# Kernel tuning notes

Measured on AMD Instinct MI355X. Metric: run time of the kernel, lower is better.

## Reference

```python
import jax, jax.numpy as jnp
import numpy as np

B, S, D, A = 8, 4096, 128, 128


def _pos_encoding(seq_len, dim):
    # sin/cos positional encoding, same construction as the torch buffer
    pos = np.arange(seq_len, dtype=np.float32)[:, None]
    div = np.exp(np.arange(0, dim, 2, dtype=np.float32) * (-np.log(10000.0) / dim))
    pe = np.zeros((seq_len, dim), dtype=np.float32)
    pe[:, 0::2] = np.sin(pos * div)
    pe[:, 1::2] = np.cos(pos * div)
    return jnp.asarray(pe)


def setup_inputs() -> dict:
    key = jax.random.key(0)
    ks = jax.random.split(key, 7)
    sc = 1.0 / np.sqrt(D)
    return {
        "x": jax.random.normal(ks[0], (B, S, D), dtype=jnp.float32),
        "Wq": jax.random.normal(ks[1], (D, A), dtype=jnp.float32) * sc,
        "bq": jnp.zeros((A,), dtype=jnp.float32),
        "Wk": jax.random.normal(ks[2], (D, A), dtype=jnp.float32) * sc,
        "bk": jnp.zeros((A,), dtype=jnp.float32),
        "Wv": jax.random.normal(ks[3], (D, A), dtype=jnp.float32) * sc,
        "bv": jnp.zeros((A,), dtype=jnp.float32),
    }


def reference(x, Wq, bq, Wk, bk, Wv, bv):
    b, s, d = x.shape
    pe = _pos_encoding(s, d)  # [S, D]
    xp = x + pe[None]  # broadcast add of positional encoding
    q = xp @ Wq + bq  # [B, S, A]
    k = xp @ Wk + bk
    v = xp @ Wv + bv
    scale = 1.0 / jnp.sqrt(jnp.asarray(Wq.shape[1], dtype=jnp.float32))
    scores = jnp.einsum("bsa,bta->bst", q, k) * scale  # [B, S, S]
    weights = jax.nn.softmax(scores, axis=-1)
    out = jnp.einsum("bst,bta->bsa", weights, v)  # [B, S, A]
    return out
```

## Files before the change

kernel.cpp:

```cpp
#include <hip/hip_runtime.h>

#define BB 8
#define SS 4096
#define DD 128

typedef __attribute__((ext_vector_type(8))) short v8s;
typedef __attribute__((ext_vector_type(4))) short v4s;
typedef __attribute__((ext_vector_type(4))) float v4f;

__device__ __forceinline__ unsigned short f2bf(float f) {
    unsigned int u = __float_as_uint(f);
    u += 0x7fffu + ((u >> 16) & 1u);
    return (unsigned short)(u >> 16);
}
__device__ __forceinline__ float bf2f(unsigned short s) {
    return __uint_as_float(((unsigned int)s) << 16);
}
__device__ __forceinline__ unsigned int pk_bf16(float a, float b) {
    unsigned int ua = __float_as_uint(a) + 0x8000u;
    unsigned int ub = __float_as_uint(b) + 0x8000u;
    return __builtin_amdgcn_perm(ub, ua, 0x07060302u);
}

#if !defined(__HIP_DEVICE_COMPILE__)
#define MFMA_BF16_32(a, b, c) (c)
#else
#define MFMA_BF16_32(a, b, c) __builtin_amdgcn_mfma_f32_16x16x32_bf16((a), (b), (c), 0, 0, 0)
#endif

#if !defined(__HIP_DEVICE_COMPILE__)
#define EXP2F(x) exp2f(x)
#elif __has_builtin(__builtin_amdgcn_exp2f)
#define EXP2F(x) __builtin_amdgcn_exp2f(x)
#else
#define EXP2F(x) exp2f(x)
#endif

#define QSCALE 0.12751743f
#define FIXM 24.0f

__global__ __launch_bounds__(256) void prep_w_kernel(
    const float* __restrict__ Wq, const float* __restrict__ Wk,
    const float* __restrict__ Wv, unsigned short* __restrict__ Wt)
{
    int id = blockIdx.x * 256 + threadIdx.x;
    int w = id >> 14;
    int n = (id >> 7) & 127;
    int k = id & 127;
    const float* W = (w == 0) ? Wq : (w == 1) ? Wk : Wv;
    Wt[id] = f2bf(W[k * 128 + n]);
}

__global__ __launch_bounds__(256) void proj_kernel(
    const float* __restrict__ x, const unsigned short* __restrict__ Wt,
    const float* __restrict__ bq, const float* __restrict__ bk,
    const float* __restrict__ bv,
    unsigned short* __restrict__ qo, unsigned short* __restrict__ ko,
    unsigned short* __restrict__ vo)
{
    __shared__ __attribute__((aligned(16))) unsigned short o_lds[9216];

    const int tid = threadIdx.x;
    const int wave = tid >> 6;
    const int lane = tid & 63;
    const int quad = lane >> 4;
    const int l15 = lane & 15;
    const int bid = blockIdx.x;
    const int mat = bid % 3;
    const int rbase = (bid / 3) * 64;

    const int flatrow = rbase + wave * 16 + l15;
    const int srow = flatrow & 4095;
    v8s af[4];
#pragma unroll
    for (int kc = 0; kc < 4; ++kc) {
        const int kbase = kc * 32 + quad * 8;
        const v4f* xp = (const v4f*)(x + (size_t)flatrow * DD + kbase);
        v4f x0 = xp[0], x1 = xp[1];
        float xv[8] = {x0[0], x0[1], x0[2], x0[3], x1[0], x1[1], x1[2], x1[3]};
        v8s a;
#pragma unroll
        for (int j = 0; j < 8; ++j) {
            int d = kbase + j;
            float freq = __expf((float)(d & ~1) * -0.07195578415606394f);
            float arg = (float)srow * freq;
            float pe = (d & 1) ? __cosf(arg) : __sinf(arg);
            a[j] = (short)f2bf(xv[j] + pe);
        }
        af[kc] = a;
    }

    const unsigned short* Wp = Wt + (mat << 14);
    const float* bias = (mat == 0) ? bq : (mat == 1) ? bk : bv;

#pragma unroll
    for (int nb = 0; nb < 8; ++nb) {
        const int col = nb * 16 + l15;
        v4f acc = {0.f, 0.f, 0.f, 0.f};
#pragma unroll
        for (int kc = 0; kc < 4; ++kc) {
            v8s bf = *(const v8s*)(Wp + col * 128 + kc * 32 + quad * 8);
            acc = MFMA_BF16_32(af[kc], bf, acc);
        }
        float bval = bias[col];
#pragma unroll
        for (int reg = 0; reg < 4; ++reg) {
            int lr = wave * 16 + quad * 4 + reg;
            float val = acc[reg] + bval;
            if (mat == 0) {
                o_lds[lr * 136 + col] = f2bf(val * QSCALE);
            } else if (mat == 1) {
                o_lds[lr * 136 + col] = f2bf(val);
            } else {
                o_lds[col * 72 + lr] = f2bf(val);
            }
        }
    }
    __syncthreads();

    if (mat <= 1) {
        unsigned short* outp = (mat == 0) ? qo : ko;
#pragma unroll
        for (int it = 0; it < 4; ++it) {
            int id = it * 256 + tid;
            int r = id >> 4, c8 = id & 15;
            *(v8s*)(outp + (size_t)(rbase + r) * DD + c8 * 8) =
                *(const v8s*)(o_lds + r * 136 + c8 * 8);
        }
    } else {
        const int b0 = rbase >> 12, s0 = rbase & 4095;
#pragma unroll
        for (int it = 0; it < 4; ++it) {
            int id = it * 256 + tid;
            int a = id >> 3, c = id & 7;
            *(v8s*)(vo + ((size_t)(b0 * 128 + a)) * SS + s0 + c * 8) =
                *(const v8s*)(o_lds + a * 72 + c * 8);
        }
    }
}

#define HKEYS 2048
#define NT (HKEYS / 64)
__global__ __launch_bounds__(256, 2) void flash_kernel(
    const unsigned short* __restrict__ qg,
    const unsigned short* __restrict__ kg,
    const unsigned short* __restrict__ vg,
    float* __restrict__ out,
    unsigned short* __restrict__ o2,
    float* __restrict__ statl)
{
    __shared__ __attribute__((aligned(16))) unsigned short k_lds[2][8192];
    __shared__ __attribute__((aligned(16))) unsigned short v_lds[2][8192];

    const int tid = threadIdx.x;
    const int wave = tid >> 6;
    const int lane = tid & 63;
    const int quad = lane >> 4;
    const int l15 = lane & 15;
    const int bid = blockIdx.x;
    const int b = bid & 7;
    const int half = (bid >> 3) & 1;
    const int qt = bid >> 4;
    const int qbase = qt * 128 + wave * 32;

    v8s qfA[4], qfB[4];
    {
        const size_t rA = (size_t)(b * SS + qbase + l15) * DD;
        const size_t rB = (size_t)(b * SS + qbase + 16 + l15) * DD;
#pragma unroll
        for (int kc = 0; kc < 4; ++kc) {
            qfA[kc] = *(const v8s*)(qg + rA + kc * 32 + quad * 8);
            qfB[kc] = *(const v8s*)(qg + rB + kc * 32 + quad * 8);
        }
    }

    v4f oA[8], oB[8];
#pragma unroll
    for (int i = 0; i < 8; ++i) {
        oA[i] = (v4f){0.f, 0.f, 0.f, 0.f};
        oB[i] = (v4f){0.f, 0.f, 0.f, 0.f};
    }
    v4f laccA = {0.f, 0.f, 0.f, 0.f}, laccB = {0.f, 0.f, 0.f, 0.f};

    v8s ones;
#pragma unroll
    for (int j = 0; j < 8; ++j) ones[j] = (short)0x3F80;

    const unsigned short* kb = kg + (size_t)b * SS * DD + (size_t)half * HKEYS * DD;
    const unsigned short* vb = vg + (size_t)b * DD * SS + half * HKEYS;

    int kbo[4], vbo[2][2];
#pragma unroll
    for (int kc = 0; kc < 4; ++kc)
        kbo[kc] = l15 * 128 + (((kc * 4 + quad) ^ (l15 & 7)) << 3);
#pragma unroll
    for (int kc2 = 0; kc2 < 2; ++kc2) {
        vbo[kc2][0] = l15 * 64 + (((kc2 * 8 + quad) ^ l15) << 2);
        vbo[kc2][1] = l15 * 64 + (((kc2 * 8 + 4 + quad) ^ l15) << 2);
    }
    const int kr_r = tid >> 4, kr_c = tid & 15;
    const int va0 = tid >> 3, vc4 = (tid & 7) * 2;
    const int kwb = kr_r * 128 + ((kr_c ^ (kr_r & 7)) << 3);
    const int vwb0 = va0 * 64 + ((vc4 ^ (va0 & 15)) << 2);
    const int vwb1 = va0 * 64 + (((vc4 + 1) ^ (va0 & 15)) << 2);

    v8s kr[4], vr[4];
    auto load_tile = [&](int t) {
        const unsigned short* kp = kb + (size_t)t * 64 * DD;
        const unsigned short* vp = vb + t * 64;
#pragma unroll
        for (int it = 0; it < 4; ++it) {
            kr[it] = *(const v8s*)(kp + (size_t)(kr_r + it * 16) * DD + kr_c * 8);
            vr[it] = *(const v8s*)(vp + (size_t)(va0 + it * 32) * SS + (tid & 7) * 8);
        }
    };
    auto store_tile = [&](int p) {
#pragma unroll
        for (int it = 0; it < 4; ++it) {
            *(v8s*)(&k_lds[p][kwb + it * 2048]) = kr[it];
            v4s lo = {vr[it][0], vr[it][1], vr[it][2], vr[it][3]};
            v4s hi = {vr[it][4], vr[it][5], vr[it][6], vr[it][7]};
            *(v4s*)(&v_lds[p][vwb0 + it * 2048]) = lo;
            *(v4s*)(&v_lds[p][vwb1 + it * 2048]) = hi;
        }
    };
    auto compute = [&](int p) {
        v4f sA[4], sB[4];
#pragma unroll
        for (int c = 0; c < 4; ++c) {
            v4f aA = {0.f, 0.f, 0.f, 0.f};
            v4f aB = {0.f, 0.f, 0.f, 0.f};
#pragma unroll
            for (int kc = 0; kc < 4; ++kc) {
                v8s af = *(const v8s*)(&k_lds[p][c * 2048 + kbo[kc]]);
                aA = MFMA_BF16_32(af, qfA[kc], aA);
                aB = MFMA_BF16_32(af, qfB[kc], aB);
            }
            sA[c] = aA;
            sB[c] = aB;
        }
        union { v8s v[2]; unsigned int u[8]; } PA, PB;
#pragma unroll
        for (int c = 0; c < 4; ++c) {
            float a0 = EXP2F(sA[c][0] - FIXM), a1 = EXP2F(sA[c][1] - FIXM);
            float a2 = EXP2F(sA[c][2] - FIXM), a3 = EXP2F(sA[c][3] - FIXM);
            PA.u[c * 2]     = pk_bf16(a0, a1);
            PA.u[c * 2 + 1] = pk_bf16(a2, a3);
            float b0 = EXP2F(sB[c][0] - FIXM), b1 = EXP2F(sB[c][1] - FIXM);
            float b2 = EXP2F(sB[c][2] - FIXM), b3 = EXP2F(sB[c][3] - FIXM);
            PB.u[c * 2]     = pk_bf16(b0, b1);
            PB.u[c * 2 + 1] = pk_bf16(b2, b3);
        }
#pragma unroll
        for (int kc2 = 0; kc2 < 2; ++kc2) {
            laccA = MFMA_BF16_32(PA.v[kc2], ones, laccA);
            laccB = MFMA_BF16_32(PB.v[kc2], ones, laccB);
#pragma unroll
            for (int ab = 0; ab < 8; ++ab) {
                union { v8s v; v4s h[2]; } bf;
                bf.h[0] = *(const v4s*)(&v_lds[p][ab * 1024 + vbo[kc2][0]]);
                bf.h[1] = *(const v4s*)(&v_lds[p][ab * 1024 + vbo[kc2][1]]);
                oA[ab] = MFMA_BF16_32(PA.v[kc2], bf.v, oA[ab]);
                oB[ab] = MFMA_BF16_32(PB.v[kc2], bf.v, oB[ab]);
            }
        }
    };

    load_tile(0);
    store_tile(0);
    load_tile(1);
    __syncthreads();
#pragma unroll 1
    for (int kt = 0; kt < NT; kt += 2) {
        store_tile(1);
        if (kt + 2 < NT) load_tile(kt + 2);
        compute(0);
        __syncthreads();
        if (kt + 2 < NT) {
            store_tile(0);
            if (kt + 3 < NT) load_tile(kt + 3);
        }
        compute(1);
        __syncthreads();
    }

    if (l15 == 0) {
        int qi = half * (BB * SS) + b * SS + qbase;
#pragma unroll
        for (int reg = 0; reg < 4; ++reg) {
            statl[qi + quad * 4 + reg] = laccA[reg];
            statl[qi + 16 + quad * 4 + reg] = laccB[reg];
        }
    }
#pragma unroll
    for (int ab = 0; ab < 8; ++ab)
#pragma unroll
        for (int reg = 0; reg < 4; ++reg) {
            int srA = qbase + quad * 4 + reg;
            size_t iA = (size_t)(b * SS + srA) * DD + ab * 16 + l15;
            size_t iB = (size_t)(b * SS + srA + 16) * DD + ab * 16 + l15;
            if (half == 0) {
                out[iA] = oA[ab][reg];
                out[iB] = oB[ab][reg];
            } else {
                o2[iA] = f2bf(oA[ab][reg]);
                o2[iB] = f2bf(oB[ab][reg]);
            }
        }
}

__global__ __launch_bounds__(256) void combine_kernel(
    float* __restrict__ out, const unsigned short* __restrict__ o2,
    const float* __restrict__ statl)
{
    int id = blockIdx.x * 256 + threadIdx.x;
    int row = id >> 5;
    int c = (id & 31) * 4;
    float l1 = statl[row], l2 = statl[BB * SS + row];
    float inv = 1.0f / (l1 + l2);
    size_t base = (size_t)row * DD + c;
    v4f o1 = *(v4f*)(out + base);
    v4s p2 = *(const v4s*)(o2 + base);
    v4f r;
#pragma unroll
    for (int j = 0; j < 4; ++j)
        r[j] = (o1[j] + bf2f((unsigned short)p2[j])) * inv;
    *(v4f*)(out + base) = r;
}

extern "C" void kernel_launch(void* const* d_in, const int* in_sizes, int n_in,
                              void* d_out, int out_size, void* d_ws, size_t ws_size,
                              hipStream_t stream)
{
    const float* x  = (const float*)d_in[0];
    const float* Wq = (const float*)d_in[1];
    const float* bq = (const float*)d_in[2];
    const float* Wk = (const float*)d_in[3];
    const float* bk = (const float*)d_in[4];
    const float* Wv = (const float*)d_in[5];
    const float* bv = (const float*)d_in[6];
    float* out = (float*)d_out;

    unsigned short* Wt = (unsigned short*)d_ws;
    unsigned short* q  = Wt + 49152;
    unsigned short* k  = q + (size_t)BB * SS * DD;
    unsigned short* vT = k + (size_t)BB * SS * DD;
    unsigned short* O2 = vT + (size_t)BB * SS * DD;
    float* statl = (float*)(O2 + (size_t)BB * SS * DD);

    hipLaunchKernelGGL(prep_w_kernel, dim3(192), dim3(256), 0, stream, Wq, Wk, Wv, Wt);
    hipLaunchKernelGGL(proj_kernel, dim3(BB * SS / 64 * 3), dim3(256), 0, stream,
                       x, Wt, bq, bk, bv, q, k, vT);
    hipLaunchKernelGGL(flash_kernel, dim3(SS / 128 * 2 * BB), dim3(256), 0, stream,
                       q, k, vT, out, O2, statl);
    hipLaunchKernelGGL(combine_kernel, dim3(BB * SS * DD / 4 / 256), dim3(256), 0, stream,
                       out, O2, statl);
}
```

Before: 187.1 us.

## Use 32x32x16 MFMA in flash attention and fuse QKV projection per block

The flash kernel moves from 16x16x32 MFMAs over 64-key tiles to 32x32x16 MFMAs over 32-key tiles. Each wave now holds one 32-row query fragment and sums row exponentials in registers with a shuffle, replacing the ones-vector MFMA used for the denominator. The projection kernel computes Q, K and V in one block, so the positional-encoded x fragment is built once instead of three times. The cost is a larger LDS footprint in the projection kernel and shorter key tiles, which means more barriers per key in the flash loop.

```diff
diff --git a/kernel.cpp b/kernel.cpp
--- a/kernel.cpp
+++ b/kernel.cpp
@@ -7,6 +7,7 @@
 typedef __attribute__((ext_vector_type(8))) short v8s;
 typedef __attribute__((ext_vector_type(4))) short v4s;
 typedef __attribute__((ext_vector_type(4))) float v4f;
+typedef __attribute__((ext_vector_type(16))) float v16f;
 
 __device__ __forceinline__ unsigned short f2bf(float f) {
     unsigned int u = __float_as_uint(f);
@@ -23,9 +24,11 @@
 }
 
 #if !defined(__HIP_DEVICE_COMPILE__)
-#define MFMA_BF16_32(a, b, c) (c)
+#define MFMA16(a, b, c) (c)
+#define MFMA32(a, b, c) (c)
 #else
-#define MFMA_BF16_32(a, b, c) __builtin_amdgcn_mfma_f32_16x16x32_bf16((a), (b), (c), 0, 0, 0)
+#define MFMA16(a, b, c) __builtin_amdgcn_mfma_f32_16x16x32_bf16((a), (b), (c), 0, 0, 0)
+#define MFMA32(a, b, c) __builtin_amdgcn_mfma_f32_32x32x16_bf16((a), (b), (c), 0, 0, 0)
 #endif
 
 #if !defined(__HIP_DEVICE_COMPILE__)
@@ -51,23 +54,23 @@
     Wt[id] = f2bf(W[k * 128 + n]);
 }
 
-__global__ __launch_bounds__(256) void proj_kernel(
+__global__ __launch_bounds__(256, 3) void proj_kernel(
     const float* __restrict__ x, const unsigned short* __restrict__ Wt,
     const float* __restrict__ bq, const float* __restrict__ bk,
     const float* __restrict__ bv,
     unsigned short* __restrict__ qo, unsigned short* __restrict__ ko,
     unsigned short* __restrict__ vo)
 {
-    __shared__ __attribute__((aligned(16))) unsigned short o_lds[9216];
+    __shared__ __attribute__((aligned(16))) unsigned short o_q[64 * 136];
+    __shared__ __attribute__((aligned(16))) unsigned short o_k[64 * 136];
+    __shared__ __attribute__((aligned(16))) unsigned short o_v[128 * 72];
 
     const int tid = threadIdx.x;
     const int wave = tid >> 6;
     const int lane = tid & 63;
     const int quad = lane >> 4;
     const int l15 = lane & 15;
-    const int bid = blockIdx.x;
-    const int mat = bid % 3;
-    const int rbase = (bid / 3) * 64;
+    const int rbase = blockIdx.x * 64;
 
     const int flatrow = rbase + wave * 16 + l15;
     const int srow = flatrow & 4095;
@@ -90,57 +93,58 @@
         af[kc] = a;
     }
 
-    const unsigned short* Wp = Wt + (mat << 14);
-    const float* bias = (mat == 0) ? bq : (mat == 1) ? bk : bv;
-
-#pragma unroll
-    for (int nb = 0; nb < 8; ++nb) {
-        const int col = nb * 16 + l15;
-        v4f acc = {0.f, 0.f, 0.f, 0.f};
-#pragma unroll
-        for (int kc = 0; kc < 4; ++kc) {
-            v8s bf = *(const v8s*)(Wp + col * 128 + kc * 32 + quad * 8);
-            acc = MFMA_BF16_32(af[kc], bf, acc);
-        }
-        float bval = bias[col];
-#pragma unroll
-        for (int reg = 0; reg < 4; ++reg) {
-            int lr = wave * 16 + quad * 4 + reg;
-            float val = acc[reg] + bval;
-            if (mat == 0) {
-                o_lds[lr * 136 + col] = f2bf(val * QSCALE);
-            } else if (mat == 1) {
-                o_lds[lr * 136 + col] = f2bf(val);
-            } else {
-                o_lds[col * 72 + lr] = f2bf(val);
+#pragma unroll
+    for (int mat = 0; mat < 3; ++mat) {
+        const unsigned short* Wp = Wt + (mat << 14);
+        const float* bias = (mat == 0) ? bq : (mat == 1) ? bk : bv;
+#pragma unroll
+        for (int nb = 0; nb < 8; ++nb) {
+            const int col = nb * 16 + l15;
+            v4f acc = {0.f, 0.f, 0.f, 0.f};
+#pragma unroll
+            for (int kc = 0; kc < 4; ++kc) {
+                v8s bf = *(const v8s*)(Wp + col * 128 + kc * 32 + quad * 8);
+                acc = MFMA16(af[kc], bf, acc);
             }
+            float bval = bias[col];
+#pragma unroll
+            for (int reg = 0; reg < 4; ++reg) {
+                int lr = wave * 16 + quad * 4 + reg;
+                float val = acc[reg] + bval;
+                if (mat == 0) {
+                    o_q[lr * 136 + col] = f2bf(val * QSCALE);
+                } else if (mat == 1) {
+                    o_k[lr * 136 + col] = f2bf(val);
+                } else {
+                    o_v[col * 72 + lr] = f2bf(val);
+                }
+            }
         }
     }
     __syncthreads();
 
-    if (mat <= 1) {
-        unsigned short* outp = (mat == 0) ? qo : ko;
-#pragma unroll
-        for (int it = 0; it < 4; ++it) {
-            int id = it * 256 + tid;
-            int r = id >> 4, c8 = id & 15;
-            *(v8s*)(outp + (size_t)(rbase + r) * DD + c8 * 8) =
-                *(const v8s*)(o_lds + r * 136 + c8 * 8);
-        }
-    } else {
-        const int b0 = rbase >> 12, s0 = rbase & 4095;
-#pragma unroll
-        for (int it = 0; it < 4; ++it) {
-            int id = it * 256 + tid;
-            int a = id >> 3, c = id & 7;
-            *(v8s*)(vo + ((size_t)(b0 * 128 + a)) * SS + s0 + c * 8) =
-                *(const v8s*)(o_lds + a * 72 + c * 8);
-        }
-    }
-}
-
+#pragma unroll
+    for (int it = 0; it < 4; ++it) {
+        int id = it * 256 + tid;
+        int r = id >> 4, c8 = id & 15;
+        *(v8s*)(qo + (size_t)(rbase + r) * DD + c8 * 8) =
+            *(const v8s*)(o_q + r * 136 + c8 * 8);
+        *(v8s*)(ko + (size_t)(rbase + r) * DD + c8 * 8) =
+            *(const v8s*)(o_k + r * 136 + c8 * 8);
+    }
+    const int b0 = rbase >> 12, s0 = rbase & 4095;
+#pragma unroll
+    for (int it = 0; it < 4; ++it) {
+        int id = it * 256 + tid;
+        int a = id >> 3, c = id & 7;
+        *(v8s*)(vo + ((size_t)(b0 * 128 + a)) * SS + s0 + c * 8) =
+            *(const v8s*)(o_v + a * 72 + c * 8);
+    }
+}
+
+#define KT 32
 #define HKEYS 2048
-#define NT (HKEYS / 64)
+#define NT (HKEYS / KT)
 __global__ __launch_bounds__(256, 2) void flash_kernel(
     const unsigned short* __restrict__ qg,
     const unsigned short* __restrict__ kg,
@@ -149,119 +153,92 @@
     unsigned short* __restrict__ o2,
     float* __restrict__ statl)
 {
-    __shared__ __attribute__((aligned(16))) unsigned short k_lds[2][8192];
-    __shared__ __attribute__((aligned(16))) unsigned short v_lds[2][8192];
+    __shared__ __attribute__((aligned(16))) unsigned short k_lds[2][KT * 128];
+    __shared__ __attribute__((aligned(16))) unsigned short v_lds[2][128 * KT];
 
     const int tid = threadIdx.x;
     const int wave = tid >> 6;
     const int lane = tid & 63;
-    const int quad = lane >> 4;
-    const int l15 = lane & 15;
+    const int hi = lane >> 5;
+    const int l31 = lane & 31;
     const int bid = blockIdx.x;
     const int b = bid & 7;
     const int half = (bid >> 3) & 1;
     const int qt = bid >> 4;
     const int qbase = qt * 128 + wave * 32;
 
-    v8s qfA[4], qfB[4];
-    {
-        const size_t rA = (size_t)(b * SS + qbase + l15) * DD;
-        const size_t rB = (size_t)(b * SS + qbase + 16 + l15) * DD;
-#pragma unroll
-        for (int kc = 0; kc < 4; ++kc) {
-            qfA[kc] = *(const v8s*)(qg + rA + kc * 32 + quad * 8);
-            qfB[kc] = *(const v8s*)(qg + rB + kc * 32 + quad * 8);
-        }
-    }
-
-    v4f oA[8], oB[8];
-#pragma unroll
-    for (int i = 0; i < 8; ++i) {
-        oA[i] = (v4f){0.f, 0.f, 0.f, 0.f};
-        oB[i] = (v4f){0.f, 0.f, 0.f, 0.f};
-    }
-    v4f laccA = {0.f, 0.f, 0.f, 0.f}, laccB = {0.f, 0.f, 0.f, 0.f};
-
-    v8s ones;
-#pragma unroll
-    for (int j = 0; j < 8; ++j) ones[j] = (short)0x3F80;
+    const size_t qrow = (size_t)(b * SS + qbase + l31) * DD;
+    v8s qf[8];
+#pragma unroll
+    for (int kc = 0; kc < 8; ++kc)
+        qf[kc] = *(const v8s*)(qg + qrow + kc * 16 + hi * 8);
+
+    v16f o[4];
+#pragma unroll
+    for (int fg = 0; fg < 4; ++fg)
+#pragma unroll
+        for (int r = 0; r < 16; ++r) o[fg][r] = 0.f;
+    float lrow = 0.f;
 
     const unsigned short* kb = kg + (size_t)b * SS * DD + (size_t)half * HKEYS * DD;
     const unsigned short* vb = vg + (size_t)b * DD * SS + half * HKEYS;
 
-    int kbo[4], vbo[2][2];
-#pragma unroll
-    for (int kc = 0; kc < 4; ++kc)
-        kbo[kc] = l15 * 128 + (((kc * 4 + quad) ^ (l15 & 7)) << 3);
-#pragma unroll
-    for (int kc2 = 0; kc2 < 2; ++kc2) {
-        vbo[kc2][0] = l15 * 64 + (((kc2 * 8 + quad) ^ l15) << 2);
-        vbo[kc2][1] = l15 * 64 + (((kc2 * 8 + 4 + quad) ^ l15) << 2);
-    }
     const int kr_r = tid >> 4, kr_c = tid & 15;
-    const int va0 = tid >> 3, vc4 = (tid & 7) * 2;
-    const int kwb = kr_r * 128 + ((kr_c ^ (kr_r & 7)) << 3);
-    const int vwb0 = va0 * 64 + ((vc4 ^ (va0 & 15)) << 2);
-    const int vwb1 = va0 * 64 + (((vc4 + 1) ^ (va0 & 15)) << 2);
-
-    v8s kr[4], vr[4];
+    const int va = tid >> 2, vc8 = tid & 3;
+    v8s kr[2], vr[2];
+
     auto load_tile = [&](int t) {
-        const unsigned short* kp = kb + (size_t)t * 64 * DD;
-        const unsigned short* vp = vb + t * 64;
-#pragma unroll
-        for (int it = 0; it < 4; ++it) {
+        const unsigned short* kp = kb + (size_t)t * KT * DD;
+        const unsigned short* vp = vb + t * KT;
+#pragma unroll
+        for (int it = 0; it < 2; ++it) {
             kr[it] = *(const v8s*)(kp + (size_t)(kr_r + it * 16) * DD + kr_c * 8);
-            vr[it] = *(const v8s*)(vp + (size_t)(va0 + it * 32) * SS + (tid & 7) * 8);
+            vr[it] = *(const v8s*)(vp + (size_t)(va + it * 64) * SS + vc8 * 8);
         }
     };
     auto store_tile = [&](int p) {
 #pragma unroll
-        for (int it = 0; it < 4; ++it) {
-            *(v8s*)(&k_lds[p][kwb + it * 2048]) = kr[it];
+        for (int it = 0; it < 2; ++it) {
+            int r = kr_r + it * 16;
+            *(v8s*)(&k_lds[p][r * 128 + ((kr_c ^ (r & 7)) << 3)]) = kr[it];
+            int a = va + it * 64;
             v4s lo = {vr[it][0], vr[it][1], vr[it][2], vr[it][3]};
-            v4s hi = {vr[it][4], vr[it][5], vr[it][6], vr[it][7]};
-            *(v4s*)(&v_lds[p][vwb0 + it * 2048]) = lo;
-            *(v4s*)(&v_lds[p][vwb1 + it * 2048]) = hi;
+            v4s hv = {vr[it][4], vr[it][5], vr[it][6], vr[it][7]};
+            int cc = vc8 >> 1, h = vc8 & 1;
+            *(v4s*)(&v_lds[p][a * 32 + (((cc ^ (a & 3)) << 3) + h * 4)]) = lo;
+            *(v4s*)(&v_lds[p][a * 32 + ((((cc + 2) ^ (a & 3)) << 3) + h * 4)]) = hv;
         }
     };
     auto compute = [&](int p) {
-        v4f sA[4], sB[4];
-#pragma unroll
-        for (int c = 0; c < 4; ++c) {
-            v4f aA = {0.f, 0.f, 0.f, 0.f};
-            v4f aB = {0.f, 0.f, 0.f, 0.f};
-#pragma unroll
-            for (int kc = 0; kc < 4; ++kc) {
-                v8s af = *(const v8s*)(&k_lds[p][c * 2048 + kbo[kc]]);
-                aA = MFMA_BF16_32(af, qfA[kc], aA);
-                aB = MFMA_BF16_32(af, qfB[kc], aB);
-            }
-            sA[c] = aA;
-            sB[c] = aB;
-        }
-        union { v8s v[2]; unsigned int u[8]; } PA, PB;
-#pragma unroll
-        for (int c = 0; c < 4; ++c) {
-            float a0 = EXP2F(sA[c][0] - FIXM), a1 = EXP2F(sA[c][1] - FIXM);
-            float a2 = EXP2F(sA[c][2] - FIXM), a3 = EXP2F(sA[c][3] - FIXM);
-            PA.u[c * 2]     = pk_bf16(a0, a1);
-            PA.u[c * 2 + 1] = pk_bf16(a2, a3);
-            float b0 = EXP2F(sB[c][0] - FIXM), b1 = EXP2F(sB[c][1] - FIXM);
-            float b2 = EXP2F(sB[c][2] - FIXM), b3 = EXP2F(sB[c][3] - FIXM);
-            PB.u[c * 2]     = pk_bf16(b0, b1);
-            PB.u[c * 2 + 1] = pk_bf16(b2, b3);
-        }
-#pragma unroll
-        for (int kc2 = 0; kc2 < 2; ++kc2) {
-            laccA = MFMA_BF16_32(PA.v[kc2], ones, laccA);
-            laccB = MFMA_BF16_32(PB.v[kc2], ones, laccB);
-#pragma unroll
-            for (int ab = 0; ab < 8; ++ab) {
-                union { v8s v; v4s h[2]; } bf;
-                bf.h[0] = *(const v4s*)(&v_lds[p][ab * 1024 + vbo[kc2][0]]);
-                bf.h[1] = *(const v4s*)(&v_lds[p][ab * 1024 + vbo[kc2][1]]);
-                oA[ab] = MFMA_BF16_32(PA.v[kc2], bf.v, oA[ab]);
-                oB[ab] = MFMA_BF16_32(PB.v[kc2], bf.v, oB[ab]);
+        v16f s;
+#pragma unroll
+        for (int r = 0; r < 16; ++r) s[r] = -FIXM;
+#pragma unroll
+        for (int kc = 0; kc < 8; ++kc) {
+            v8s af = *(const v8s*)(&k_lds[p][l31 * 128 +
+                                   (((kc * 2 + hi) ^ (l31 & 7)) << 3)]);
+            s = MFMA32(af, qf[kc], s);
+        }
+        float e[16];
+#pragma unroll
+        for (int r = 0; r < 16; ++r) {
+            e[r] = EXP2F(s[r]);
+            lrow += e[r];
+        }
+        union { v8s v[2]; unsigned int u[8]; } P;
+#pragma unroll
+        for (int g = 0; g < 2; ++g)
+#pragma unroll
+            for (int m = 0; m < 4; ++m)
+                P.u[g * 4 + m] = pk_bf16(e[2 * m + 8 * g], e[2 * m + 8 * g + 1]);
+#pragma unroll
+        for (int fg = 0; fg < 4; ++fg) {
+            int row = fg * 32 + l31;
+#pragma unroll
+            for (int g = 0; g < 2; ++g) {
+                v8s bf = *(const v8s*)(&v_lds[p][row * 32 +
+                                       (((2 * hi + g) ^ (row & 3)) << 3)]);
+                o[fg] = MFMA32(P.v[g], bf, o[fg]);
             }
         }
     };
@@ -284,28 +261,17 @@
         __syncthreads();
     }
 
-    if (l15 == 0) {
-        int qi = half * (BB * SS) + b * SS + qbase;
-#pragma unroll
-        for (int reg = 0; reg < 4; ++reg) {
-            statl[qi + quad * 4 + reg] = laccA[reg];
-            statl[qi + 16 + quad * 4 + reg] = laccB[reg];
-        }
-    }
-#pragma unroll
-    for (int ab = 0; ab < 8; ++ab)
-#pragma unroll
-        for (int reg = 0; reg < 4; ++reg) {
-            int srA = qbase + quad * 4 + reg;
-            size_t iA = (size_t)(b * SS + srA) * DD + ab * 16 + l15;
-            size_t iB = (size_t)(b * SS + srA + 16) * DD + ab * 16 + l15;
-            if (half == 0) {
-                out[iA] = oA[ab][reg];
-                out[iB] = oB[ab][reg];
-            } else {
-                o2[iA] = f2bf(oA[ab][reg]);
-                o2[iB] = f2bf(oB[ab][reg]);
-            }
+    lrow += __shfl_xor(lrow, 32, 64);
+    if (lane < 32)
+        statl[half * (BB * SS) + b * SS + qbase + l31] = lrow;
+#pragma unroll
+    for (int fg = 0; fg < 4; ++fg)
+#pragma unroll
+        for (int r = 0; r < 16; ++r) {
+            int qr = (r & 3) + 8 * (r >> 2) + 4 * hi;
+            size_t idx = (size_t)(b * SS + qbase + qr) * DD + fg * 32 + l31;
+            if (half == 0) out[idx] = o[fg][r];
+            else           o2[idx] = f2bf(o[fg][r]);
         }
 }
 
@@ -349,7 +315,7 @@
     float* statl = (float*)(O2 + (size_t)BB * SS * DD);
 
     hipLaunchKernelGGL(prep_w_kernel, dim3(192), dim3(256), 0, stream, Wq, Wk, Wv, Wt);
-    hipLaunchKernelGGL(proj_kernel, dim3(BB * SS / 64 * 3), dim3(256), 0, stream,
+    hipLaunchKernelGGL(proj_kernel, dim3(BB * SS / 64), dim3(256), 0, stream,
                        x, Wt, bq, bk, bv, q, k, vT);
     hipLaunchKernelGGL(flash_kernel, dim3(SS / 128 * 2 * BB), dim3(256), 0, stream,
                        q, k, vT, out, O2, statl);
```

Result: no change. 187.9 us (+0.5%).
